# Performance work log

Hardware: AMD Instinct MI355X
Metric: run time of the kernel (lower is better)

## Reference

```python
import jax, jax.numpy as jnp
import numpy as np

N_NODES = 4096   # nodes 0..N-1; node 0 = source, node N-1 = sink
FAN_IN = 4096    # fixed number of incoming edges per non-source node


def setup_inputs() -> dict:
    key = jax.random.key(0)
    N, K = N_NODES, FAN_IN
    j = np.arange(1, N, dtype=np.int64)[:, None]          # [N-1,1] end nodes
    t = np.arange(K, dtype=np.int64)[None, :]              # [1,K] pred offsets
    starts = np.maximum(j - 1 - t, 0)                      # [N-1,K] clamp pads to node 0
    ends = np.broadcast_to(j, starts.shape)
    gold = np.broadcast_to((t == 0).astype(np.int64), starts.shape)  # gold path 0->1->...->N-1
    graph = np.ascontiguousarray(
        np.stack([starts, ends, gold], axis=-1).reshape(-1, 3))      # [E,3]
    weight = jax.random.normal(key, (graph.shape[0],), dtype=jnp.float32)
    return {"graph": jnp.asarray(graph), "weight": weight}


def _forward_alg(graph_path, weight):
    # Edges are grouped by end node (topological id order), FAN_IN per node.
    N, K = N_NODES, FAN_IN
    preds = graph_path[:, 0].reshape(N - 1, K)   # [N-1,K] predecessor node ids
    w = weight.reshape(N - 1, K)                 # [N-1,K] edge weights

    def step(esum, inp):
        j, p_j, w_j = inp
        # esum[end] = logsumexp over incoming edges of (esum[start] - weight)
        e_j = jax.nn.logsumexp(esum[p_j] - w_j)
        return esum.at[j].set(e_j), None

    esum0 = jnp.zeros((N,), weight.dtype)        # esum[0] = 0 (source)
    nodes = jnp.arange(1, N)
    esum, _ = jax.lax.scan(step, esum0, (nodes, preds, w))
    return esum[-1]


def reference(graph, weight):
    mask = graph[:, 2].astype(weight.dtype)
    gold_score = jnp.sum(weight * mask)
    gp = graph[:, :2]
    gp = gp - gp.min()                           # matches graph_path - graph_path.min()
    forward_score = _forward_alg(gp, weight)
    return gold_score + forward_score
```

## Files before the change

kernel.cpp:

```cpp
#include <hip/hip_runtime.h>
#include <math.h>

#define NN 4096
#define KK 4096
#define RR 4095
#define TPB 1024
#define TILE 32
#define NWORK 128
#define NTAIL 16

__device__ __forceinline__ float rdlane(float v, int l) {
  return __int_as_float(__builtin_amdgcn_readlane(__float_as_int(v), l));
}

__global__ void __launch_bounds__(TPB) fused_kernel(const float* __restrict__ w,
                                                    float* __restrict__ out) {
  const int T = blockIdx.x;
  const int t0 = (T > 1) ? (T - 1) : 0;
  const int LT = T - t0 + 1;
  const int base = TILE * t0;

  __shared__ float es[2 * TILE + 1];
  __shared__ float Tri[2][TILE][TILE + 1];
  __shared__ float U[2][TILE];
  __shared__ float refs[2];
  __shared__ float tlS[NTAIL];

  const int tid = threadIdx.x;
  const int lane = tid & 63, wid = tid >> 6;
  const int lo0 = 1 + base;

  if (tid == 0) { refs[0] = 0.f; refs[1] = 0.f; }

  float greg = 0.f;
  if (wid == 0) {
    const int jg = 1 + TILE * T + lane;
    if (lane < TILE && jg < NN) greg = w[(size_t)(jg - 1) * KK];
  }

  {
    const int l = tid >> 5, c = tid & 31;
    const int j = lo0 + l;
    float a = 0.f;
    if (c < l && j < NN) a = __expf(-w[(size_t)(j - 1) * KK + (l - 1 - c)]);
    Tri[0][l][c] = a;
  }

  if (t0 == 0) {
    const int j = wid + 1;
    const float4* row4 = (const float4*)(w + (size_t)(j - 1) * KK);
    const int tmin = j - 1;
    float s0, s1, s2, s3;
    {
      const float4 v = row4[lane];
      const int tb = 4 * lane;
      s0 = (tb + 0 >= tmin) ? __expf(-v.x) : 0.f;
      s1 = (tb + 1 >= tmin) ? __expf(-v.y) : 0.f;
      s2 = (tb + 2 >= tmin) ? __expf(-v.z) : 0.f;
      s3 = (tb + 3 >= tmin) ? __expf(-v.w) : 0.f;
    }
    #pragma unroll
    for (int c = 1; c < 16; ++c) {
      const float4 v = row4[lane + 64 * c];
      s0 += __expf(-v.x); s1 += __expf(-v.y);
      s2 += __expf(-v.z); s3 += __expf(-v.w);
    }
    float S = (s0 + s1) + (s2 + s3);
    #pragma unroll
    for (int off = 1; off < 64; off <<= 1) S += __shfl_xor(S, off);
    if (lane == 0) tlS[wid] = S;
  }
  __syncthreads();
  if (tid < TILE)
    U[0][tid] = (t0 == 0) ? ((tid < NTAIL) ? tlS[tid] : 0.f) : 1.f;
  __syncthreads();

  for (int tau = 0; tau < LT; ++tau) {
    const int tg = t0 + tau;
    const int lo = 1 + TILE * tg;
    const bool more = (tau + 1 < LT);
    const int lo_n = lo + TILE;

    float bwv = 1e30f, trv = 1e30f;
    int jrow = NN;
    if (more) {
      const int l = wid * 2 + (lane >> 5);
      const int c = lane & 31;
      const int j = lo_n + l;
      jrow = j;
      const int jc = (j < NN) ? j : RR;
      bwv = w[(size_t)(jc - 1) * KK + (jc - 1) - (lo + c)];
      const int l2 = tid >> 5, c2 = tid & 31;
      const int j2 = lo_n + l2;
      const int j2c = (j2 < NN) ? j2 : RR;
      const float v = w[(size_t)(j2c - 1) * KK + ((c2 < l2) ? (l2 - 1 - c2) : 0)];
      trv = (c2 < l2 && j2 < NN) ? v : 1e30f;
    }
    __builtin_amdgcn_sched_barrier(0);

    if (wid == 0) {
      const float ref = refs[tau & 1];
      float acc = (lane < TILE) ? U[tau & 1][lane] : 0.f;
      float lsc = 0.f;
      #pragma unroll
      for (int g = 0; g < 4; ++g) {
        const int c0 = g * 8;
        float av[8];
        #pragma unroll
        for (int u2 = 0; u2 < 8; ++u2) av[u2] = Tri[tau & 1][lane & 31][c0 + u2];
        #pragma unroll
        for (int u2 = 0; u2 < 8; ++u2) {
          const float xc = rdlane(acc, c0 + u2);
          acc = fmaf(av[u2], xc, acc);
        }
        if (g == 1) {
          const float sc = rdlane(acc, c0 + 7);
          if (sc > 1e18f) { acc *= 1.f / sc; lsc += __logf(sc); }
        }
      }
      const float e = ref + lsc + __logf(acc);
      const int j = lo + lane;
      if (lane < TILE && j < NN) es[j - base] = e;
      if (lane == TILE - 1) refs[(tau + 1) & 1] = e;
    }
    __syncthreads();

    if (more) {
      const float ref_n = refs[(tau + 1) & 1];
      const int c = lane & 31;
      const float yv = __expf(es[1 + TILE * tau + c] - ref_n);
      float acc = yv * __expf(-bwv);
      #pragma unroll
      for (int off = 1; off < 32; off <<= 1) acc += __shfl_xor(acc, off);
      if ((lane & 31) == 0) {
        const int l = wid * 2 + (lane >> 5);
        U[(tau + 1) & 1][l] = (jrow < NN) ? acc : 0.f;
      }
      const int l2 = tid >> 5, c2 = tid & 31;
      Tri[(tau + 1) & 1][l2][c2] = __expf(-trv);
    }
    __syncthreads();
  }

  if (wid == 0) {
    #pragma unroll
    for (int off = 1; off < 64; off <<= 1) greg += __shfl_xor(greg, off);
    if (lane == 0) {
      const int qLO = (T == NWORK - 1) ? (TILE * LT - 1) : (TILE * LT);
      float delta = es[qLO] + greg;
      if (T >= 1) delta -= es[TILE * (LT - 1)];
      atomicAdd(out, delta);
    }
  }
}

extern "C" void kernel_launch(void* const* d_in, const int* in_sizes, int n_in,
                              void* d_out, int out_size, void* d_ws, size_t ws_size,
                              hipStream_t stream) {
  (void)in_sizes; (void)n_in; (void)out_size; (void)d_ws; (void)ws_size;
  (void)d_in[0];
  const float* weight = (const float*)d_in[1];
  float* out = (float*)d_out;

  hipMemsetAsync((void*)out, 0, sizeof(float), stream);

  hipLaunchKernelGGL(fused_kernel, dim3(NWORK), dim3(TPB), 0, stream,
                     weight, out);
}
```

Before: 15.86 us.

## Replace two-tile pipelined solve with a single 64-wide triangular window per block

Each block now builds one 64x64 lower-triangular transfer matrix covering its warm-up tile and its own tile, then runs a single 64-step forward substitution in one wavefront. This removes the per-tile loop with its boundary-weight gathers, shared-memory handoffs and several block-wide barriers. The trade-off is a longer serial readlane/FMA chain in one wave (64 steps instead of two 32-step solves) and rescaling at two checkpoints, which could affect numerical range.

```diff
diff --git a/kernel.cpp b/kernel.cpp
--- a/kernel.cpp
+++ b/kernel.cpp
@@ -6,6 +6,7 @@
 #define RR 4095
 #define TPB 1024
 #define TILE 32
+#define WIN 64
 #define NWORK 128
 #define NTAIL 16
 
@@ -16,37 +17,32 @@
 __global__ void __launch_bounds__(TPB) fused_kernel(const float* __restrict__ w,
                                                     float* __restrict__ out) {
   const int T = blockIdx.x;
-  const int t0 = (T > 1) ? (T - 1) : 0;
-  const int LT = T - t0 + 1;
-  const int base = TILE * t0;
+  const int s = (T >= 1) ? TILE * (T - 1) : 0;
+  const bool anchor = (T <= 1);
 
-  __shared__ float es[2 * TILE + 1];
-  __shared__ float Tri[2][TILE][TILE + 1];
-  __shared__ float U[2][TILE];
-  __shared__ float refs[2];
+  __shared__ float Tri[WIN][WIN + 1];
   __shared__ float tlS[NTAIL];
 
   const int tid = threadIdx.x;
   const int lane = tid & 63, wid = tid >> 6;
-  const int lo0 = 1 + base;
-
-  if (tid == 0) { refs[0] = 0.f; refs[1] = 0.f; }
 
   float greg = 0.f;
-  if (wid == 0) {
+  if (wid == 0 && lane < TILE) {
     const int jg = 1 + TILE * T + lane;
-    if (lane < TILE && jg < NN) greg = w[(size_t)(jg - 1) * KK];
+    if (jg < NN) greg = w[(size_t)(jg - 1) * KK];
   }
 
-  {
-    const int l = tid >> 5, c = tid & 31;
-    const int j = lo0 + l;
+  #pragma unroll
+  for (int q = 0; q < 4; ++q) {
+    const int idx = tid + TPB * q;
+    const int l = idx >> 6, c = idx & 63;
+    const int j = s + 1 + l;
     float a = 0.f;
     if (c < l && j < NN) a = __expf(-w[(size_t)(j - 1) * KK + (l - 1 - c)]);
-    Tri[0][l][c] = a;
+    Tri[l][c] = a;
   }
 
-  if (t0 == 0) {
+  if (anchor) {
     const int j = wid + 1;
     const float4* row4 = (const float4*)(w + (size_t)(j - 1) * KK);
     const int tmin = j - 1;
@@ -71,84 +67,38 @@
     if (lane == 0) tlS[wid] = S;
   }
   __syncthreads();
-  if (tid < TILE)
-    U[0][tid] = (t0 == 0) ? ((tid < NTAIL) ? tlS[tid] : 0.f) : 1.f;
-  __syncthreads();
-
-  for (int tau = 0; tau < LT; ++tau) {
-    const int tg = t0 + tau;
-    const int lo = 1 + TILE * tg;
-    const bool more = (tau + 1 < LT);
-    const int lo_n = lo + TILE;
-
-    float bwv = 1e30f, trv = 1e30f;
-    int jrow = NN;
-    if (more) {
-      const int l = wid * 2 + (lane >> 5);
-      const int c = lane & 31;
-      const int j = lo_n + l;
-      jrow = j;
-      const int jc = (j < NN) ? j : RR;
-      bwv = w[(size_t)(jc - 1) * KK + (jc - 1) - (lo + c)];
-      const int l2 = tid >> 5, c2 = tid & 31;
-      const int j2 = lo_n + l2;
-      const int j2c = (j2 < NN) ? j2 : RR;
-      const float v = w[(size_t)(j2c - 1) * KK + ((c2 < l2) ? (l2 - 1 - c2) : 0)];
-      trv = (c2 < l2 && j2 < NN) ? v : 1e30f;
-    }
-    __builtin_amdgcn_sched_barrier(0);
-
-    if (wid == 0) {
-      const float ref = refs[tau & 1];
-      float acc = (lane < TILE) ? U[tau & 1][lane] : 0.f;
-      float lsc = 0.f;
-      #pragma unroll
-      for (int g = 0; g < 4; ++g) {
-        const int c0 = g * 8;
-        float av[8];
-        #pragma unroll
-        for (int u2 = 0; u2 < 8; ++u2) av[u2] = Tri[tau & 1][lane & 31][c0 + u2];
-        #pragma unroll
-        for (int u2 = 0; u2 < 8; ++u2) {
-          const float xc = rdlane(acc, c0 + u2);
-          acc = fmaf(av[u2], xc, acc);
-        }
-        if (g == 1) {
-          const float sc = rdlane(acc, c0 + 7);
-          if (sc > 1e18f) { acc *= 1.f / sc; lsc += __logf(sc); }
-        }
-      }
-      const float e = ref + lsc + __logf(acc);
-      const int j = lo + lane;
-      if (lane < TILE && j < NN) es[j - base] = e;
-      if (lane == TILE - 1) refs[(tau + 1) & 1] = e;
-    }
-    __syncthreads();
-
-    if (more) {
-      const float ref_n = refs[(tau + 1) & 1];
-      const int c = lane & 31;
-      const float yv = __expf(es[1 + TILE * tau + c] - ref_n);
-      float acc = yv * __expf(-bwv);
-      #pragma unroll
-      for (int off = 1; off < 32; off <<= 1) acc += __shfl_xor(acc, off);
-      if ((lane & 31) == 0) {
-        const int l = wid * 2 + (lane >> 5);
-        U[(tau + 1) & 1][l] = (jrow < NN) ? acc : 0.f;
-      }
-      const int l2 = tid >> 5, c2 = tid & 31;
-      Tri[(tau + 1) & 1][l2][c2] = __expf(-trv);
-    }
-    __syncthreads();
-  }
 
   if (wid == 0) {
+    float acc = anchor ? ((lane < NTAIL) ? tlS[lane] : 0.f) : 1.f;
+    float lsc = 0.f;
+    #pragma unroll
+    for (int g = 0; g < 8; ++g) {
+      const int c0 = g * 8;
+      float av[8];
+      #pragma unroll
+      for (int u2 = 0; u2 < 8; ++u2) av[u2] = Tri[lane][c0 + u2];
+      #pragma unroll
+      for (int u2 = 0; u2 < 8; ++u2) {
+        const float xc = rdlane(acc, c0 + u2);
+        acc = fmaf(av[u2], xc, acc);
+      }
+      if (g == 3 || g == 5) {
+        const float sc = rdlane(acc, c0 + 7);
+        if (sc > 1e18f) { acc *= 1.f / sc; lsc += __logf(sc); }
+      }
+    }
+    const float e = lsc + __logf(acc);
+
     #pragma unroll
     for (int off = 1; off < 64; off <<= 1) greg += __shfl_xor(greg, off);
+
+    const float eLW = rdlane(e, TILE - 1);
+    const int loLane = (T == 0) ? (TILE - 1)
+                     : ((T == NWORK - 1) ? (WIN - 2) : (WIN - 1));
+    const float eLO = rdlane(e, loLane);
     if (lane == 0) {
-      const int qLO = (T == NWORK - 1) ? (TILE * LT - 1) : (TILE * LT);
-      float delta = es[qLO] + greg;
-      if (T >= 1) delta -= es[TILE * (LT - 1)];
+      float delta = eLO + greg;
+      if (T >= 1) delta -= eLW;
       atomicAdd(out, delta);
     }
   }
```

After: 16.10 us. About the same (+1.5%).
